# Kernel optimization log

Hardware: AMD Instinct MI355X
Metric: run time of the kernel (lower is better)

Reference implementation:

```python
import jax, jax.numpy as jnp
import numpy as np

B = 64; H = 64; W = 64; C = 128
NH = 4; WS = 4; SHIFT = 2
N = WS * WS; HD = C // NH; SCALE = HD ** -0.5
HID = 4 * C; EPS = 1e-6


def _rel_index():
    # faithful to source: meshgrid(coords_w, coords_h, indexing='ij'); hard-coded 4 == WS
    coords = np.stack(np.meshgrid(np.arange(WS), np.arange(WS), indexing='ij')).reshape(2, -1)
    rel = coords[:, :, None] - coords[:, None, :]
    rel = rel.transpose(1, 2, 0).copy()
    rel[:, :, 0] += WS - 1
    rel[:, :, 1] += WS - 1
    rel[:, :, 0] *= 2 * WS - 1
    return rel.sum(-1)  # (N, N) int

REL_IDX = jnp.asarray(_rel_index())


def _attn_mask():
    img = np.zeros((H, W))
    sl = (slice(0, -WS), slice(-WS, -SHIFT), slice(-SHIFT, None))
    cnt = 0
    for hs in sl:
        for ws_ in sl:
            img[hs, ws_] = cnt
            cnt += 1
    mw = img.reshape(H // WS, WS, W // WS, WS).transpose(0, 2, 1, 3).reshape(-1, N)
    m = mw[:, None, :] - mw[:, :, None]  # (nW, N, N)
    return jnp.asarray(np.where(m != 0, -100.0, 0.0).astype(np.float32))

MASK = _attn_mask()  # (nW, N, N)


def _ln(x, s, b):
    mu = x.mean(-1, keepdims=True)
    var = ((x - mu) ** 2).mean(-1, keepdims=True)
    return (x - mu) * jax.lax.rsqrt(var + EPS) * s + b


def setup_inputs() -> dict:
    key = jax.random.key(0)
    ks = jax.random.split(key, 8)
    def nrm(k, shape, scale=0.02):
        return jax.random.normal(k, shape, jnp.float32) * scale
    return dict(
        x=jax.random.normal(ks[0], (B, H * W, C), jnp.float32),
        ln1_scale=jnp.ones((C,), jnp.float32), ln1_bias=jnp.zeros((C,), jnp.float32),
        qkv_w=nrm(ks[1], (C, 3 * C)), qkv_b=jnp.zeros((3 * C,), jnp.float32),
        rel_bias=nrm(ks[2], ((2 * WS - 1) ** 2, NH)),
        proj_w=nrm(ks[3], (C, C)), proj_b=jnp.zeros((C,), jnp.float32),
        ln2_scale=jnp.ones((C,), jnp.float32), ln2_bias=jnp.zeros((C,), jnp.float32),
        fc1_w=nrm(ks[4], (C, HID)), fc1_b=jnp.zeros((HID,), jnp.float32),
        fc2_w=nrm(ks[5], (HID, C)), fc2_b=jnp.zeros((C,), jnp.float32),
    )


def reference(x, ln1_scale, ln1_bias, qkv_w, qkv_b, rel_bias, proj_w, proj_b,
              ln2_scale, ln2_bias, fc1_w, fc1_b, fc2_w, fc2_b):
    shortcut = x
    h = _ln(x, ln1_scale, ln1_bias).reshape(B, H, W, C)
    h = jnp.roll(h, (-SHIFT, -SHIFT), axis=(1, 2))
    # window partition -> (B*nW, N, C)
    xw = h.reshape(B, H // WS, WS, W // WS, WS, C).transpose(0, 1, 3, 2, 4, 5).reshape(-1, N, C)
    B_ = xw.shape[0]
    qkv = (xw @ qkv_w + qkv_b).reshape(B_, N, 3, NH, HD).transpose(2, 0, 3, 1, 4)
    q, k, v = qkv[0] * SCALE, qkv[1], qkv[2]
    attn = jnp.einsum('bhnd,bhmd->bhnm', q, k)  # (B_, NH, N, N)
    bias = rel_bias[REL_IDX.reshape(-1)].reshape(N, N, NH).transpose(2, 0, 1)
    attn = attn + bias[None]
    nW = MASK.shape[0]
    attn = attn.reshape(B_ // nW, nW, NH, N, N) + MASK[None, :, None]
    attn = jax.nn.softmax(attn.reshape(B_, NH, N, N), axis=-1)
    attn = jax.nn.softmax(attn, axis=-1)  # source applies softmax twice when mask is present
    out = jnp.einsum('bhnm,bhmd->bhnd', attn, v).transpose(0, 2, 1, 3).reshape(B_, N, C)
    out = out @ proj_w + proj_b
    # window reverse
    h = out.reshape(B, H // WS, W // WS, WS, WS, C).transpose(0, 1, 3, 2, 4, 5).reshape(B, H, W, C)
    h = jnp.roll(h, (SHIFT, SHIFT), axis=(1, 2)).reshape(B, H * W, C)
    x = shortcut + h
    m = _ln(x, ln2_scale, ln2_bias)
    m = jax.nn.gelu(m @ fc1_w + fc1_b) @ fc2_w + fc2_b  # flax nn.gelu default approximate=True
    return x + m
```

## Files before the change

kernel.cpp:

```cpp
#include <hip/hip_runtime.h>

typedef __bf16 bf16x8 __attribute__((ext_vector_type(8)));
typedef __bf16 bf16x4 __attribute__((ext_vector_type(4)));
typedef float f32x4 __attribute__((ext_vector_type(4)));
typedef unsigned short us8 __attribute__((ext_vector_type(8)));
typedef unsigned short us4 __attribute__((ext_vector_type(4)));
typedef short sh4 __attribute__((ext_vector_type(4)));

#define SCALE_Q 0.17677669529663687f

__device__ __forceinline__ unsigned short f2b(float f) {
    __bf16 h = (__bf16)f;
    return __builtin_bit_cast(unsigned short, h);
}
__device__ __forceinline__ float b2f(unsigned short h) {
    union { unsigned u; float f; } v; v.u = ((unsigned)h) << 16;
    return v.f;
}
__device__ __forceinline__ f32x4 mfma16(us8 a, us8 b, f32x4 c) {
    return __builtin_amdgcn_mfma_f32_16x16x32_bf16(
        __builtin_bit_cast(bf16x8, a), __builtin_bit_cast(bf16x8, b), c, 0, 0, 0);
}

#if __has_builtin(__builtin_amdgcn_mfma_f32_16x16x16bf16_1k)
__device__ __forceinline__ f32x4 mfma16k16(us4 a, us4 b, f32x4 c) {
    return __builtin_amdgcn_mfma_f32_16x16x16bf16_1k(
        __builtin_bit_cast(sh4, a), __builtin_bit_cast(sh4, b), c, 0, 0, 0);
}
#elif __has_builtin(__builtin_amdgcn_mfma_f32_16x16x16_bf16)
__device__ __forceinline__ f32x4 mfma16k16(us4 a, us4 b, f32x4 c) {
    return __builtin_amdgcn_mfma_f32_16x16x16_bf16(
        __builtin_bit_cast(bf16x4, a), __builtin_bit_cast(bf16x4, b), c, 0, 0, 0);
}
#else
__device__ __forceinline__ f32x4 mfma16k16(us4 a, us4 b, f32x4 c) {
    asm volatile("v_mfma_f32_16x16x16_bf16 %0, %1, %2, %0"
                 : "+v"(c) : "v"(a), "v"(b));
    return c;
}
#endif

__device__ __forceinline__ us8 lds_ld8(const unsigned short* base, int byteoff) {
    return *(const us8*)((const char*)base + byteoff);
}
__device__ __forceinline__ void lds_st8(unsigned short* base, int byteoff, us8 v) {
    *(us8*)((char*)base + byteoff) = v;
}

__global__ void k_pack_qkvw(const float* __restrict__ qkv_w, unsigned short* __restrict__ dst) {
    int gid = blockIdx.x * 256 + threadIdx.x;
    int blk = gid >> 9, rem = gid & 511;
    int lane = rem >> 3, j = rem & 7;
    int cc = blk >> 2, kk = blk & 3;
    int col = cc * 16 + (lane & 15);
    int k = kk * 32 + (lane >> 4) * 8 + j;
    float v = qkv_w[k * 384 + col];
    if (col < 128) v *= SCALE_Q;
    dst[gid] = f2b(v);
}
__global__ void k_scale_qkvb(const float* __restrict__ qkv_b, float* __restrict__ dst) {
    int i = blockIdx.x * 256 + threadIdx.x;
    if (i < 384) dst[i] = qkv_b[i] * (i < 128 ? SCALE_Q : 1.f);
}
__global__ void k_pack_projw(const float* __restrict__ proj_w, unsigned short* __restrict__ dst) {
    int gid = blockIdx.x * 256 + threadIdx.x;
    int blk = gid >> 9, rem = gid & 511;
    int lane = rem >> 3, j = rem & 7;
    int cc = blk >> 2, kk = blk & 3;
    int col = cc * 16 + (lane & 15);
    int k = kk * 32 + (lane >> 4) * 8 + j;
    dst[gid] = f2b(proj_w[k * 128 + col]);
}

__global__ void k_pack_mlp(const float* __restrict__ fc1_w, const float* __restrict__ fc2_w,
                           unsigned short* __restrict__ wPack) {
    int gid = blockIdx.x * 256 + threadIdx.x;
    int pair = gid >> 13;
    int rem = gid & 8191;
    float v;
    if (rem < 4096) {
        int half = rem >> 11;
        int r2 = rem & 2047;
        int kk = r2 >> 9, r3 = r2 & 511;
        int lane = r3 >> 3, j = r3 & 7;
        int m = lane & 15;
        int col = pair * 32 + (m >> 2) * 8 + half * 4 + (m & 3);
        int k = kk * 32 + (lane >> 4) * 8 + j;
        v = fc1_w[(size_t)k * 512 + col];
    } else {
        int r2 = rem - 4096;
        int co = r2 >> 9, r3 = r2 & 511;
        int lane = r3 >> 3, j = r3 & 7;
        int k = pair * 32 + (lane >> 4) * 8 + j;
        v = fc2_w[(size_t)k * 128 + co * 16 + (lane & 15)];
    }
    wPack[gid] = f2b(v);
}

__global__ __launch_bounds__(256, 3) void k_block1(
    const float* __restrict__ x,
    const float* __restrict__ ln1s, const float* __restrict__ ln1b,
    const unsigned short* __restrict__ qkvWp, const float* __restrict__ qkvBs,
    const float* __restrict__ relb,
    const unsigned short* __restrict__ projWp, const float* __restrict__ projB,
    unsigned short* __restrict__ xmid)
{
    __shared__ unsigned short sm[4 * 6144];
    __shared__ float sbias[196];
    const int tid = threadIdx.x;
    const int wave = tid >> 6, lane = tid & 63;
    const int g = lane >> 4, m16 = lane & 15;
    if (tid < 196) sbias[tid] = relb[tid];
    const int win0 = blockIdx.x * 4;
    const int winM = win0 + wave;
    const int bbM = winM >> 8, whM = (winM >> 4) & 15, wnM = winM & 15;

    {
        float4 sc0 = *(const float4*)(ln1s + m16 * 8);
        float4 sc1 = *(const float4*)(ln1s + m16 * 8 + 4);
        float4 bi0 = *(const float4*)(ln1b + m16 * 8);
        float4 bi1 = *(const float4*)(ln1b + m16 * 8 + 4);
        #pragma unroll
        for (int it = 0; it < 4; ++it) {
            int tok = it * 4 + g;
            int ti = tok >> 2, tj = tok & 3;
            int hh = (whM * 4 + ti + 2) & 63, ww = (wnM * 4 + tj + 2) & 63;
            const float* xr = x + ((((size_t)bbM << 12) | (hh << 6) | ww) * 128) + m16 * 8;
            float4 v0 = *(const float4*)xr, v1 = *(const float4*)(xr + 4);
            float sum = v0.x + v0.y + v0.z + v0.w + v1.x + v1.y + v1.z + v1.w;
            float sq  = v0.x*v0.x + v0.y*v0.y + v0.z*v0.z + v0.w*v0.w
                      + v1.x*v1.x + v1.y*v1.y + v1.z*v1.z + v1.w*v1.w;
            #pragma unroll
            for (int m = 1; m < 16; m <<= 1) { sum += __shfl_xor(sum, m); sq += __shfl_xor(sq, m); }
            float mu = sum * 0.0078125f;
            float rstd = rsqrtf(sq * 0.0078125f - mu * mu + 1e-6f);
            us8 o;
            o[0] = f2b((v0.x - mu) * rstd * sc0.x + bi0.x);
            o[1] = f2b((v0.y - mu) * rstd * sc0.y + bi0.y);
            o[2] = f2b((v0.z - mu) * rstd * sc0.z + bi0.z);
            o[3] = f2b((v0.w - mu) * rstd * sc0.w + bi0.w);
            o[4] = f2b((v1.x - mu) * rstd * sc1.x + bi1.x);
            o[5] = f2b((v1.y - mu) * rstd * sc1.y + bi1.y);
            o[6] = f2b((v1.z - mu) * rstd * sc1.z + bi1.z);
            o[7] = f2b((v1.w - mu) * rstd * sc1.w + bi1.w);
            lds_st8(sm, wave * 12288 + tok * 256 + ((m16 * 16) ^ ((tok & 7) << 4)), o);
        }
    }
    __syncthreads();

    us8 afr[4][4];
    #pragma unroll
    for (int w = 0; w < 4; ++w)
        #pragma unroll
        for (int k = 0; k < 4; ++k)
            afr[w][k] = lds_ld8(sm, w * 12288 + m16 * 256 + ((k * 64 + g * 16) ^ ((m16 & 7) << 4)));
    __syncthreads();

    #pragma unroll
    for (int ct = 0; ct < 6; ++ct) {
        const unsigned short* bp = qkvWp + (size_t)((wave * 6 + ct) * 4) * 512 + lane * 8;
        us8 b0 = *(const us8*)(bp);
        us8 b1 = *(const us8*)(bp + 512);
        us8 b2 = *(const us8*)(bp + 1024);
        us8 b3 = *(const us8*)(bp + 1536);
        const int cb = wave * 96 + ct * 16;
        const int s = cb >> 7;
        if (s == 2) {
            f32x4 acc[4] = {{0.f,0.f,0.f,0.f},{0.f,0.f,0.f,0.f},{0.f,0.f,0.f,0.f},{0.f,0.f,0.f,0.f}};
            #pragma unroll
            for (int w = 0; w < 4; ++w) {
                acc[w] = mfma16(afr[w][0], b0, acc[w]);
                acc[w] = mfma16(afr[w][1], b1, acc[w]);
                acc[w] = mfma16(afr[w][2], b2, acc[w]);
                acc[w] = mfma16(afr[w][3], b3, acc[w]);
            }
            const int c = cb + m16;
            const float bias = qkvBs[c];
            const int rem = c & 127, hq = rem >> 5, hd = rem & 31;
            #pragma unroll
            for (int w = 0; w < 4; ++w) {
                us4 pk;
                #pragma unroll
                for (int jj = 0; jj < 4; ++jj) pk[jj] = f2b(acc[w][jj] + bias);
                *(us4*)((char*)sm + w * 12288 + 8192 + hq * 1024 + hd * 32
                        + ((g ^ ((hd >> 2) & 3)) << 3)) = pk;
            }
        } else {
            f32x4 acc[4] = {{0.f,0.f,0.f,0.f},{0.f,0.f,0.f,0.f},{0.f,0.f,0.f,0.f},{0.f,0.f,0.f,0.f}};
            #pragma unroll
            for (int w = 0; w < 4; ++w) {
                acc[w] = mfma16(b0, afr[w][0], acc[w]);
                acc[w] = mfma16(b1, afr[w][1], acc[w]);
                acc[w] = mfma16(b2, afr[w][2], acc[w]);
                acc[w] = mfma16(b3, afr[w][3], acc[w]);
            }
            const int cb4 = cb + g * 4;
            float4 b4 = *(const float4*)(qkvBs + cb4);
            const int rem = cb4 & 127, hq = rem >> 5, hd0 = rem & 31;
            const int chunk = (hd0 >> 3) ^ ((m16 >> 1) & 3);
            const int off = s * 4096 + hq * 1024 + m16 * 64 + chunk * 16 + (hd0 & 7) * 2;
            #pragma unroll
            for (int w = 0; w < 4; ++w) {
                us4 pk;
                pk[0] = f2b(acc[w][0] + b4.x);
                pk[1] = f2b(acc[w][1] + b4.y);
                pk[2] = f2b(acc[w][2] + b4.z);
                pk[3] = f2b(acc[w][3] + b4.w);
                *(us4*)((char*)sm + w * 12288 + off) = pk;
            }
        }
    }
    __syncthreads();

    {
        const int base = wave * 12288;
        const int ti = m16 >> 2, tj = m16 & 3;
        const int hhq = whM * 4 + ti, wwq = wnM * 4 + tj;
        const int myid = (hhq < 60 ? 0 : (hhq < 62 ? 3 : 6)) + (wwq < 60 ? 0 : (wwq < 62 ? 1 : 2));
        const int qkswz = (g ^ ((m16 >> 1) & 3)) * 16;
        const int vswz  = (g ^ ((m16 >> 2) & 3)) << 3;
        f32x4 po[4][2];
        #pragma unroll
        for (int h = 0; h < 4; ++h) {
            us8 kf = lds_ld8(sm, base + 4096 + h * 1024 + m16 * 64 + qkswz);
            us8 qf = lds_ld8(sm, base +        h * 1024 + m16 * 64 + qkswz);
            f32x4 st = mfma16(kf, qf, (f32x4){0.f,0.f,0.f,0.f});
            float p[4];
            #pragma unroll
            for (int jj = 0; jj < 4; ++jj) {
                int kk = g * 4 + jj;
                int pi = kk >> 2, pj = kk & 3;
                int hhk = whM * 4 + pi, wwk = wnM * 4 + pj;
                int pid = (hhk < 60 ? 0 : (hhk < 62 ? 3 : 6)) + (wwk < 60 ? 0 : (wwk < 62 ? 1 : 2));
                float v = st[jj] + sbias[((ti - pi + 3) * 7 + (tj - pj + 3)) * 4 + h];
                p[jj] = (pid != myid) ? v - 100.f : v;
            }
            #pragma unroll
            for (int rep = 0; rep < 2; ++rep) {
                float mx = fmaxf(fmaxf(p[0], p[1]), fmaxf(p[2], p[3]));
                mx = fmaxf(mx, __shfl_xor(mx, 16));
                mx = fmaxf(mx, __shfl_xor(mx, 32));
                float ssum = 0.f;
                #pragma unroll
                for (int jj = 0; jj < 4; ++jj) { p[jj] = __expf(p[jj] - mx); ssum += p[jj]; }
                ssum += __shfl_xor(ssum, 16);
                ssum += __shfl_xor(ssum, 32);
                float inv = 1.f / ssum;
                #pragma unroll
                for (int jj = 0; jj < 4; ++jj) p[jj] *= inv;
            }
            us4 pf;
            #pragma unroll
            for (int jj = 0; jj < 4; ++jj) pf[jj] = f2b(p[jj]);
            #pragma unroll
            for (int dh = 0; dh < 2; ++dh) {
                us4 vf = *(const us4*)((const char*)sm + base + 8192 + h * 1024
                                       + (dh * 16 + m16) * 32 + vswz);
                po[h][dh] = mfma16k16(vf, pf, (f32x4){0.f,0.f,0.f,0.f});
            }
        }
        #pragma unroll
        for (int h = 0; h < 4; ++h)
            #pragma unroll
            for (int dh = 0; dh < 2; ++dh) {
                us4 pk;
                #pragma unroll
                for (int jj = 0; jj < 4; ++jj) pk[jj] = f2b(po[h][dh][jj]);
                *(us4*)((char*)sm + base + m16 * 256
                        + ((h * 64 + dh * 32 + g * 8) ^ ((m16 & 7) << 4))) = pk;
            }
    }
    __syncthreads();

    {
        us8 cfr[4][4];
        #pragma unroll
        for (int w = 0; w < 4; ++w)
            #pragma unroll
            for (int k = 0; k < 4; ++k)
                cfr[w][k] = lds_ld8(sm, w * 12288 + m16 * 256 + ((k * 64 + g * 16) ^ ((m16 & 7) << 4)));
        #pragma unroll
        for (int ct = 0; ct < 2; ++ct) {
            const unsigned short* bp = projWp + (size_t)((wave * 2 + ct) * 4) * 512 + lane * 8;
            us8 b0 = *(const us8*)(bp);
            us8 b1 = *(const us8*)(bp + 512);
            us8 b2 = *(const us8*)(bp + 1024);
            us8 b3 = *(const us8*)(bp + 1536);
            const int cb4 = wave * 32 + ct * 16 + g * 4;
            float4 pb4 = *(const float4*)(projB + cb4);
            #pragma unroll
            for (int w = 0; w < 4; ++w) {
                f32x4 acc = {0.f, 0.f, 0.f, 0.f};
                acc = mfma16(b0, cfr[w][0], acc);
                acc = mfma16(b1, cfr[w][1], acc);
                acc = mfma16(b2, cfr[w][2], acc);
                acc = mfma16(b3, cfr[w][3], acc);
                const int winw = win0 + w;
                const int bb = winw >> 8, wh = (winw >> 4) & 15, wn = winw & 15;
                const int tok = m16;
                int hh3 = (wh * 4 + (tok >> 2) + 2) & 63;
                int ww3 = (wn * 4 + (tok & 3) + 2) & 63;
                size_t t = (((size_t)bb << 12) | (hh3 << 6) | ww3);
                float4 xr = *(const float4*)(x + t * 128 + cb4);
                us4 pk;
                pk[0] = f2b(acc[0] + pb4.x + xr.x);
                pk[1] = f2b(acc[1] + pb4.y + xr.y);
                pk[2] = f2b(acc[2] + pb4.z + xr.z);
                pk[3] = f2b(acc[3] + pb4.w + xr.w);
                *(us4*)(xmid + t * 128 + cb4) = pk;
            }
        }
    }
}

__global__ __launch_bounds__(256, 3) void k_block2(
    const unsigned short* __restrict__ xmid,
    float* __restrict__ out,
    const float* __restrict__ ln2s, const float* __restrict__ ln2b,
    const unsigned short* __restrict__ wPack,
    const float* __restrict__ fc1B, const float* __restrict__ fc2B)
{
    __shared__ unsigned short smem[24576];
    const int tid = threadIdx.x;
    const int wave = tid >> 6, lane = tid & 63;
    const int g = lane >> 4, m16 = lane & 15;
    const size_t r0 = (size_t)blockIdx.x * 128;
    unsigned short* scr = &smem[wave * 2048];

    #pragma unroll
    for (int sub = 0; sub < 4; ++sub) {
        const unsigned short* src = wPack + sub * 2048 + tid * 8;
        unsigned short* dst = &smem[8192 + sub * 2048 + wave * 512];
#if __has_builtin(__builtin_amdgcn_global_load_lds)
        __builtin_amdgcn_global_load_lds(
            (const __attribute__((address_space(1))) void*)src,
            (__attribute__((address_space(3))) void*)dst, 16, 0, 0);
#else
        *(us8*)(dst + lane * 8) = *(const us8*)src;
#endif
    }

    float scv[8], biv[8];
    {
        float4 s0 = *(const float4*)(ln2s + m16 * 8);
        float4 s1 = *(const float4*)(ln2s + m16 * 8 + 4);
        float4 b0 = *(const float4*)(ln2b + m16 * 8);
        float4 b1 = *(const float4*)(ln2b + m16 * 8 + 4);
        scv[0]=s0.x; scv[1]=s0.y; scv[2]=s0.z; scv[3]=s0.w;
        scv[4]=s1.x; scv[5]=s1.y; scv[6]=s1.z; scv[7]=s1.w;
        biv[0]=b0.x; biv[1]=b0.y; biv[2]=b0.z; biv[3]=b0.w;
        biv[4]=b1.x; biv[5]=b1.y; biv[6]=b1.z; biv[7]=b1.w;
    }
    us8 bx[2][4];
    #pragma unroll
    for (int rt = 0; rt < 2; ++rt) {
        #pragma unroll
        for (int it = 0; it < 4; ++it) {
            int lr = it * 4 + g;
            us8 u = *(const us8*)(xmid + (r0 + wave * 32 + rt * 16 + lr) * 128 + m16 * 8);
            float f[8];
            #pragma unroll
            for (int q = 0; q < 8; ++q) f[q] = b2f(u[q]);
            float sum = 0.f, sq = 0.f;
            #pragma unroll
            for (int q = 0; q < 8; ++q) { sum += f[q]; sq += f[q] * f[q]; }
            #pragma unroll
            for (int m = 1; m < 16; m <<= 1) { sum += __shfl_xor(sum, m); sq += __shfl_xor(sq, m); }
            float mu = sum * 0.0078125f;
            float rstd = rsqrtf(sq * 0.0078125f - mu * mu + 1e-6f);
            us8 o;
            #pragma unroll
            for (int q = 0; q < 8; ++q) o[q] = f2b((f[q] - mu) * rstd * scv[q] + biv[q]);
            lds_st8(scr, lr * 256 + ((m16 * 16) ^ ((lr & 7) << 4)), o);
        }
        #pragma unroll
        for (int kk = 0; kk < 4; ++kk)
            bx[rt][kk] = lds_ld8(scr, m16 * 256 + ((kk * 64 + g * 16) ^ ((m16 & 7) << 4)));
    }
    __syncthreads();

    f32x4 accO[2][8];
    #pragma unroll
    for (int rt = 0; rt < 2; ++rt)
        #pragma unroll
        for (int co = 0; co < 8; ++co) accO[rt][co] = (f32x4){0.f, 0.f, 0.f, 0.f};

    for (int p = 0; p < 16; ++p) {
        if (p < 15) {
            #pragma unroll
            for (int sub = 0; sub < 4; ++sub) {
                const unsigned short* src = wPack + (p + 1) * 8192 + sub * 2048 + tid * 8;
                unsigned short* dst = &smem[8192 + ((p + 1) & 1) * 8192 + sub * 2048 + wave * 512];
#if __has_builtin(__builtin_amdgcn_global_load_lds)
                __builtin_amdgcn_global_load_lds(
                    (const __attribute__((address_space(1))) void*)src,
                    (__attribute__((address_space(3))) void*)dst, 16, 0, 0);
#else
                *(us8*)(dst + lane * 8) = *(const us8*)src;
#endif
            }
        }
        const char* wb = (const char*)&smem[8192 + (p & 1) * 8192];
        f32x4 hA0 = {0.f,0.f,0.f,0.f}, hA1 = {0.f,0.f,0.f,0.f};
        #pragma unroll
        for (int kk = 0; kk < 4; ++kk) {
            us8 aw = *(const us8*)(wb + kk * 1024 + lane * 16);
            hA0 = mfma16(aw, bx[0][kk], hA0);
            hA1 = mfma16(aw, bx[1][kk], hA1);
        }
        f32x4 hB0 = {0.f,0.f,0.f,0.f}, hB1 = {0.f,0.f,0.f,0.f};
        #pragma unroll
        for (int kk = 0; kk < 4; ++kk) {
            us8 aw = *(const us8*)(wb + 4096 + kk * 1024 + lane * 16);
            hB0 = mfma16(aw, bx[0][kk], hB0);
            hB1 = mfma16(aw, bx[1][kk], hB1);
        }
        float4 bA = *(const float4*)(fc1B + p * 32 + g * 8);
        float4 bB = *(const float4*)(fc1B + p * 32 + g * 8 + 4);
        us8 pa0, pa1;
        #pragma unroll
        for (int jj = 0; jj < 4; ++jj) {
            float v0 = hA0[jj] + ((const float*)&bA)[jj];
            float z0 = v0 + 0.044715f * v0 * v0 * v0;
            pa0[jj] = f2b(v0 * __builtin_amdgcn_rcpf(1.f + __builtin_amdgcn_exp2f(-2.3022082f * z0)));
            float w0 = hB0[jj] + ((const float*)&bB)[jj];
            float y0 = w0 + 0.044715f * w0 * w0 * w0;
            pa0[4 + jj] = f2b(w0 * __builtin_amdgcn_rcpf(1.f + __builtin_amdgcn_exp2f(-2.3022082f * y0)));
            float v1 = hA1[jj] + ((const float*)&bA)[jj];
            float z1 = v1 + 0.044715f * v1 * v1 * v1;
            pa1[jj] = f2b(v1 * __builtin_amdgcn_rcpf(1.f + __builtin_amdgcn_exp2f(-2.3022082f * z1)));
            float w1 = hB1[jj] + ((const float*)&bB)[jj];
            float y1 = w1 + 0.044715f * w1 * w1 * w1;
            pa1[4 + jj] = f2b(w1 * __builtin_amdgcn_rcpf(1.f + __builtin_amdgcn_exp2f(-2.3022082f * y1)));
        }
        #pragma unroll
        for (int co = 0; co < 8; ++co) {
            us8 bw = *(const us8*)(wb + 8192 + co * 1024 + lane * 16);
            accO[0][co] = mfma16(pa0, bw, accO[0][co]);
            accO[1][co] = mfma16(pa1, bw, accO[1][co]);
        }
        __syncthreads();
    }

    #pragma unroll
    for (int rt = 0; rt < 2; ++rt)
        #pragma unroll
        for (int co = 0; co < 8; ++co) {
            int col = co * 16 + m16;
            float b2v = fc2B[col];
            #pragma unroll
            for (int jj = 0; jj < 4; ++jj) {
                size_t row = r0 + wave * 32 + rt * 16 + g * 4 + jj;
                out[row * 128 + col] = accO[rt][co][jj] + b2v + b2f(xmid[row * 128 + col]);
            }
        }
}

extern "C" void kernel_launch(void* const* d_in, const int* in_sizes, int n_in,
                              void* d_out, int out_size, void* d_ws, size_t ws_size,
                              hipStream_t stream) {
    const float* x        = (const float*)d_in[0];
    const float* ln1_s    = (const float*)d_in[1];
    const float* ln1_b    = (const float*)d_in[2];
    const float* qkv_w    = (const float*)d_in[3];
    const float* qkv_b    = (const float*)d_in[4];
    const float* rel_bias = (const float*)d_in[5];
    const float* proj_w   = (const float*)d_in[6];
    const float* proj_b   = (const float*)d_in[7];
    const float* ln2_s    = (const float*)d_in[8];
    const float* ln2_b    = (const float*)d_in[9];
    const float* fc1_w    = (const float*)d_in[10];
    const float* fc1_b    = (const float*)d_in[11];
    const float* fc2_w    = (const float*)d_in[12];
    const float* fc2_b    = (const float*)d_in[13];
    float* out = (float*)d_out;
    char* ws = (char*)d_ws;

    unsigned short* qkv_wp  = (unsigned short*)(ws);
    unsigned short* proj_wp = (unsigned short*)(ws + 98304);
    unsigned short* wpack   = (unsigned short*)(ws + 131072);
    float*          qkv_bs  = (float*)(ws + 393216);
    unsigned short* xmid    = (unsigned short*)(ws + 524288);

    k_pack_qkvw<<<192, 256, 0, stream>>>(qkv_w, qkv_wp);
    k_scale_qkvb<<<2, 256, 0, stream>>>(qkv_b, qkv_bs);
    k_pack_projw<<<64, 256, 0, stream>>>(proj_w, proj_wp);
    k_pack_mlp<<<512, 256, 0, stream>>>(fc1_w, fc2_w, wpack);

    k_block1<<<4096, 256, 0, stream>>>(x, ln1_s, ln1_b, qkv_wp, qkv_bs, rel_bias,
                                       proj_wp, proj_b, xmid);
    k_block2<<<2048, 256, 0, stream>>>(xmid, out, ln2_s, ln2_b, wpack, fc1_b, fc2_b);
}
```

Measured before the change: 210.9 us.

## Split block1 work across eight waves per block instead of four

k_block1 now launches with 512 threads (eight waves) per block, and each window's work is split between two waves. Each wave handles half the tokens for LN1, three qkv column tiles instead of six, two heads in attention, and four projection column tiles for its own window. Per-wave register pressure drops (po arrays and cfr[4][4] are removed), which allows more resident waves and more latency hiding. The cost is more waves competing for LDS bandwidth and barrier synchronization across eight waves.

New measurement: 225.9 us. 1.07x slower.

```diff
diff --git a/kernel.cpp b/kernel.cpp
--- a/kernel.cpp
+++ b/kernel.cpp
@@ -97,7 +97,7 @@
     wPack[gid] = f2b(v);
 }
 
-__global__ __launch_bounds__(256, 3) void k_block1(
+__global__ __launch_bounds__(512, 4) void k_block1(
     const float* __restrict__ x,
     const float* __restrict__ ln1s, const float* __restrict__ ln1b,
     const unsigned short* __restrict__ qkvWp, const float* __restrict__ qkvBs,
@@ -111,8 +111,9 @@
     const int wave = tid >> 6, lane = tid & 63;
     const int g = lane >> 4, m16 = lane & 15;
     if (tid < 196) sbias[tid] = relb[tid];
+    const int pw = wave >> 1, half = wave & 1;
     const int win0 = blockIdx.x * 4;
-    const int winM = win0 + wave;
+    const int winM = win0 + pw;
     const int bbM = winM >> 8, whM = (winM >> 4) & 15, wnM = winM & 15;
 
     {
@@ -121,8 +122,8 @@
         float4 bi0 = *(const float4*)(ln1b + m16 * 8);
         float4 bi1 = *(const float4*)(ln1b + m16 * 8 + 4);
         #pragma unroll
-        for (int it = 0; it < 4; ++it) {
-            int tok = it * 4 + g;
+        for (int it = 0; it < 2; ++it) {
+            int tok = half * 8 + it * 4 + g;
             int ti = tok >> 2, tj = tok & 3;
             int hh = (whM * 4 + ti + 2) & 63, ww = (wnM * 4 + tj + 2) & 63;
             const float* xr = x + ((((size_t)bbM << 12) | (hh << 6) | ww) * 128) + m16 * 8;
@@ -143,7 +144,7 @@
             o[5] = f2b((v1.y - mu) * rstd * sc1.y + bi1.y);
             o[6] = f2b((v1.z - mu) * rstd * sc1.z + bi1.z);
             o[7] = f2b((v1.w - mu) * rstd * sc1.w + bi1.w);
-            lds_st8(sm, wave * 12288 + tok * 256 + ((m16 * 16) ^ ((tok & 7) << 4)), o);
+            lds_st8(sm, pw * 12288 + tok * 256 + ((m16 * 16) ^ ((tok & 7) << 4)), o);
         }
     }
     __syncthreads();
@@ -157,14 +158,14 @@
     __syncthreads();
 
     #pragma unroll
-    for (int ct = 0; ct < 6; ++ct) {
-        const unsigned short* bp = qkvWp + (size_t)((wave * 6 + ct) * 4) * 512 + lane * 8;
+    for (int i = 0; i < 3; ++i) {
+        const int cc = wave * 3 + i;
+        const unsigned short* bp = qkvWp + (size_t)(cc * 4) * 512 + lane * 8;
         us8 b0 = *(const us8*)(bp);
         us8 b1 = *(const us8*)(bp + 512);
         us8 b2 = *(const us8*)(bp + 1024);
         us8 b3 = *(const us8*)(bp + 1536);
-        const int cb = wave * 96 + ct * 16;
-        const int s = cb >> 7;
+        const int s = cc >> 3;
         if (s == 2) {
             f32x4 acc[4] = {{0.f,0.f,0.f,0.f},{0.f,0.f,0.f,0.f},{0.f,0.f,0.f,0.f},{0.f,0.f,0.f,0.f}};
             #pragma unroll
@@ -174,7 +175,7 @@
                 acc[w] = mfma16(afr[w][2], b2, acc[w]);
                 acc[w] = mfma16(afr[w][3], b3, acc[w]);
             }
-            const int c = cb + m16;
+            const int c = cc * 16 + m16;
             const float bias = qkvBs[c];
             const int rem = c & 127, hq = rem >> 5, hd = rem & 31;
             #pragma unroll
@@ -194,7 +195,7 @@
                 acc[w] = mfma16(b2, afr[w][2], acc[w]);
                 acc[w] = mfma16(b3, afr[w][3], acc[w]);
             }
-            const int cb4 = cb + g * 4;
+            const int cb4 = cc * 16 + g * 4;
             float4 b4 = *(const float4*)(qkvBs + cb4);
             const int rem = cb4 & 127, hq = rem >> 5, hd0 = rem & 31;
             const int chunk = (hd0 >> 3) ^ ((m16 >> 1) & 3);
@@ -213,15 +214,15 @@
     __syncthreads();
 
     {
-        const int base = wave * 12288;
+        const int base = pw * 12288;
         const int ti = m16 >> 2, tj = m16 & 3;
         const int hhq = whM * 4 + ti, wwq = wnM * 4 + tj;
         const int myid = (hhq < 60 ? 0 : (hhq < 62 ? 3 : 6)) + (wwq < 60 ? 0 : (wwq < 62 ? 1 : 2));
         const int qkswz = (g ^ ((m16 >> 1) & 3)) * 16;
         const int vswz  = (g ^ ((m16 >> 2) & 3)) << 3;
-        f32x4 po[4][2];
-        #pragma unroll
-        for (int h = 0; h < 4; ++h) {
+        #pragma unroll
+        for (int hi = 0; hi < 2; ++hi) {
+            const int h = half * 2 + hi;
             us8 kf = lds_ld8(sm, base + 4096 + h * 1024 + m16 * 64 + qkswz);
             us8 qf = lds_ld8(sm, base +        h * 1024 + m16 * 64 + qkswz);
             f32x4 st = mfma16(kf, qf, (f32x4){0.f,0.f,0.f,0.f});
@@ -256,59 +257,48 @@
             for (int dh = 0; dh < 2; ++dh) {
                 us4 vf = *(const us4*)((const char*)sm + base + 8192 + h * 1024
                                        + (dh * 16 + m16) * 32 + vswz);
-                po[h][dh] = mfma16k16(vf, pf, (f32x4){0.f,0.f,0.f,0.f});
-            }
-        }
-        #pragma unroll
-        for (int h = 0; h < 4; ++h)
-            #pragma unroll
-            for (int dh = 0; dh < 2; ++dh) {
+                f32x4 po = mfma16k16(vf, pf, (f32x4){0.f,0.f,0.f,0.f});
                 us4 pk;
                 #pragma unroll
-                for (int jj = 0; jj < 4; ++jj) pk[jj] = f2b(po[h][dh][jj]);
+                for (int jj = 0; jj < 4; ++jj) pk[jj] = f2b(po[jj]);
                 *(us4*)((char*)sm + base + m16 * 256
                         + ((h * 64 + dh * 32 + g * 8) ^ ((m16 & 7) << 4))) = pk;
             }
+        }
     }
     __syncthreads();
 
     {
-        us8 cfr[4][4];
-        #pragma unroll
-        for (int w = 0; w < 4; ++w)
-            #pragma unroll
-            for (int k = 0; k < 4; ++k)
-                cfr[w][k] = lds_ld8(sm, w * 12288 + m16 * 256 + ((k * 64 + g * 16) ^ ((m16 & 7) << 4)));
-        #pragma unroll
-        for (int ct = 0; ct < 2; ++ct) {
-            const unsigned short* bp = projWp + (size_t)((wave * 2 + ct) * 4) * 512 + lane * 8;
+        us8 cfr[4];
+        #pragma unroll
+        for (int k = 0; k < 4; ++k)
+            cfr[k] = lds_ld8(sm, pw * 12288 + m16 * 256 + ((k * 64 + g * 16) ^ ((m16 & 7) << 4)));
+        const int tok = m16;
+        int hh3 = (whM * 4 + (tok >> 2) + 2) & 63;
+        int ww3 = (wnM * 4 + (tok & 3) + 2) & 63;
+        size_t t = (((size_t)bbM << 12) | (hh3 << 6) | ww3);
+        #pragma unroll
+        for (int i = 0; i < 4; ++i) {
+            const int ct = half * 4 + i;
+            const unsigned short* bp = projWp + (size_t)(ct * 4) * 512 + lane * 8;
             us8 b0 = *(const us8*)(bp);
             us8 b1 = *(const us8*)(bp + 512);
             us8 b2 = *(const us8*)(bp + 1024);
             us8 b3 = *(const us8*)(bp + 1536);
-            const int cb4 = wave * 32 + ct * 16 + g * 4;
+            const int cb4 = ct * 16 + g * 4;
             float4 pb4 = *(const float4*)(projB + cb4);
-            #pragma unroll
-            for (int w = 0; w < 4; ++w) {
-                f32x4 acc = {0.f, 0.f, 0.f, 0.f};
-                acc = mfma16(b0, cfr[w][0], acc);
-                acc = mfma16(b1, cfr[w][1], acc);
-                acc = mfma16(b2, cfr[w][2], acc);
-                acc = mfma16(b3, cfr[w][3], acc);
-                const int winw = win0 + w;
-                const int bb = winw >> 8, wh = (winw >> 4) & 15, wn = winw & 15;
-                const int tok = m16;
-                int hh3 = (wh * 4 + (tok >> 2) + 2) & 63;
-                int ww3 = (wn * 4 + (tok & 3) + 2) & 63;
-                size_t t = (((size_t)bb << 12) | (hh3 << 6) | ww3);
-                float4 xr = *(const float4*)(x + t * 128 + cb4);
-                us4 pk;
-                pk[0] = f2b(acc[0] + pb4.x + xr.x);
-                pk[1] = f2b(acc[1] + pb4.y + xr.y);
-                pk[2] = f2b(acc[2] + pb4.z + xr.z);
-                pk[3] = f2b(acc[3] + pb4.w + xr.w);
-                *(us4*)(xmid + t * 128 + cb4) = pk;
-            }
+            f32x4 acc = {0.f, 0.f, 0.f, 0.f};
+            acc = mfma16(b0, cfr[0], acc);
+            acc = mfma16(b1, cfr[1], acc);
+            acc = mfma16(b2, cfr[2], acc);
+            acc = mfma16(b3, cfr[3], acc);
+            float4 xr = *(const float4*)(x + t * 128 + cb4);
+            us4 pk;
+            pk[0] = f2b(acc[0] + pb4.x + xr.x);
+            pk[1] = f2b(acc[1] + pb4.y + xr.y);
+            pk[2] = f2b(acc[2] + pb4.z + xr.z);
+            pk[3] = f2b(acc[3] + pb4.w + xr.w);
+            *(us4*)(xmid + t * 128 + cb4) = pk;
         }
     }
 }
@@ -487,7 +477,7 @@
     k_pack_projw<<<64, 256, 0, stream>>>(proj_w, proj_wp);
     k_pack_mlp<<<512, 256, 0, stream>>>(fc1_w, fc2_w, wpack);
 
-    k_block1<<<4096, 256, 0, stream>>>(x, ln1_s, ln1_b, qkv_wp, qkv_bs, rel_bias,
+    k_block1<<<4096, 512, 0, stream>>>(x, ln1_s, ln1_b, qkv_wp, qkv_bs, rel_bias,
                                        proj_wp, proj_b, xmid);
     k_block2<<<2048, 256, 0, stream>>>(xmid, out, ln2_s, ln2_b, wpack, fc1_b, fc2_b);
 }
```
